# Performance work log

Hardware: AMD Instinct MI355X
Metric: run time of the kernel (lower is better)

Reference implementation:

```python
import jax, jax.numpy as jnp
import numpy as np

B, C, H, W = 16, 64, 1024, 16  # requires C*W == H per the module's implicit view/matmul constraint
C8 = C // 8


def setup_inputs() -> dict:
    key = jax.random.key(0)
    ks = jax.random.split(key, 7)
    s_in = 1.0 / np.sqrt(C)
    return {
        "x": jax.random.normal(ks[0], (B, C, H, W), dtype=jnp.float32),
        "Wq": jax.random.normal(ks[1], (C8, C), dtype=jnp.float32) * s_in,
        "bq": jax.random.normal(ks[2], (C8,), dtype=jnp.float32) * 0.01,
        "Wk": jax.random.normal(ks[3], (C8, C), dtype=jnp.float32) * s_in,
        "bk": jax.random.normal(ks[4], (C8,), dtype=jnp.float32) * 0.01,
        "Wv": jax.random.normal(ks[5], (C, C), dtype=jnp.float32) * s_in,
        "bv": jax.random.normal(ks[6], (C,), dtype=jnp.float32) * 0.01,
    }


def conv1x1(x, w, b):
    # 1x1 conv == per-pixel channel mixing: [B,C,H,W] x [O,C] -> [B,O,H,W]
    return jnp.einsum("bchw,oc->bohw", x, w) + b[None, :, None, None]


def reference(x, Wq, bq, Wk, bk, Wv, bv):
    b, c, h, w = x.shape
    q = conv1x1(x, Wq, bq)  # [B, C/8, H, W]
    k = conv1x1(x, Wk, bk)  # [B, C/8, H, W]
    v = conv1x1(x, Wv, bv)  # [B, C, H, W]
    # Faithful to torch .view(B, -1, H): row-major reshape, NOT a transpose.
    qf = jnp.swapaxes(q.reshape(b, -1, h), 1, 2)  # [B, H, C8*W]
    kf = k.reshape(b, -1, h)                      # [B, C8*W, H]
    vf = v.reshape(b, -1, h)                      # [B, C*W, H] (C*W == H)
    scores = jax.nn.softmax(jnp.matmul(qf, kf), axis=-1)  # [B, H, H]
    attended = jnp.matmul(scores, vf)             # [B, H, H]
    attended = attended.reshape(v.shape)          # [B, C, H, W]
    return x + attended
```

## Files before the change

kernel.cpp:

```cpp
#include <hip/hip_runtime.h>
#include <stdint.h>

typedef uint32_t u32;
typedef __attribute__((ext_vector_type(4))) float f32x4;
typedef __attribute__((ext_vector_type(8))) short short8;

#define NBATCH 16
#define NPIX   16384
#define NPB    1048576

__device__ __forceinline__ ushort f2bf(float f) {
  u32 b = __builtin_bit_cast(u32, f);
  return (ushort)((b + 0x7FFFu + ((b >> 16) & 1u)) >> 16);
}
__device__ __forceinline__ float bf2f(ushort h) {
  return __builtin_bit_cast(float, (u32)h << 16);
}

__device__ __forceinline__ void gload16(const void* g, void* l) {
  __builtin_amdgcn_global_load_lds(
      (const __attribute__((address_space(1))) u32*)g,
      (__attribute__((address_space(3))) u32*)l,
      16, 0, 0);
}

__global__ void prep_w2(const float* __restrict__ Wq, const float* __restrict__ bq,
                        const float* __restrict__ Wk, const float* __restrict__ bk,
                        const float* __restrict__ Wv, const float* __restrict__ bv,
                        ushort* __restrict__ Wpk, float* __restrict__ bpk)
{
  int gid = blockIdx.x * 256 + threadIdx.x;
  if (gid < 12288) {
    int m = gid >> 7, kk = gid & 127;
    int ch = kk & 63;
    ushort outv = 0;
    if (m < 8) {
      float wv = Wq[m * 64 + ch];
      ushort h = f2bf(wv);
      outv = (kk < 64) ? h : f2bf(wv - bf2f(h));
    } else if (m < 16) {
      float wv = Wk[(m - 8) * 64 + ch];
      ushort h = f2bf(wv);
      outv = (kk < 64) ? h : f2bf(wv - bf2f(h));
    } else if (m < 80) {
      outv = (kk < 64) ? f2bf(Wv[(m - 16) * 64 + ch]) : (ushort)0;
    }
    Wpk[gid] = outv;
  } else if (gid < 12368) {
    int o = gid - 12288;
    bpk[o] = (o < 8) ? bq[o] : (o < 16 ? bk[o - 8] : bv[o - 16]);
  }
}

__global__ __launch_bounds__(256) void proj10(
    const float* __restrict__ x, const ushort* __restrict__ Wpk,
    const float* __restrict__ bpk,
    ushort* __restrict__ Qt2, ushort* __restrict__ Kt2,
    ushort* __restrict__ Vt)
{
  __shared__ __align__(16) char smem[32768];
  float* xs = (float*)smem;
  int t = threadIdx.x;
  int w = t >> 6, lane = t & 63;
  int l15 = lane & 15, l4 = lane >> 4;

  int g = blockIdx.x;
  int lin = (g & 7) * 256 + (g >> 3);
  int b = lin >> 7;
  int l0 = (lin & 127) << 3;
  const float* xb = x + (size_t)b * NPB + l0;

  #pragma unroll
  for (int it = 0; it < 8; ++it) {
    int f0 = (it * 4 + w) * 64;
    int f = f0 + lane;
    int ch = f >> 5, r2 = f & 31, tc = r2 >> 1, half = r2 & 1;
    gload16(xb + (size_t)ch * NPIX + tc * 1024 + half * 4, xs + f0 * 4);
  }

  const uint4* Wp4 = (const uint4*)Wpk;
  uint4 Afrag[12];
  #pragma unroll
  for (int kc = 0; kc < 4; ++kc)
    Afrag[kc] = Wp4[l15 * 16 + kc * 4 + l4];
  #pragma unroll
  for (int mt = 1; mt < 5; ++mt)
    #pragma unroll
    for (int kc = 0; kc < 2; ++kc)
      Afrag[2 + mt * 2 + kc] = Wp4[(mt * 16 + l15) * 16 + kc * 4 + l4];

  f32x4 acc[5][2];
  #pragma unroll
  for (int mt = 0; mt < 5; ++mt) {
    f32x4 bv4;
    #pragma unroll
    for (int r = 0; r < 4; ++r) bv4[r] = bpk[mt * 16 + l4 * 4 + r];
    acc[mt][0] = bv4; acc[mt][1] = bv4;
  }

  __syncthreads();

  #pragma unroll
  for (int i = 0; i < 2; ++i) {
    int px = (w * 2 + i) * 16 + l15;
    u32 xr[16];
    #pragma unroll
    for (int kc = 0; kc < 2; ++kc)
      #pragma unroll
      for (int j = 0; j < 8; ++j)
        xr[kc * 8 + j] = ((const u32*)xs)[(kc * 32 + l4 * 8 + j) * 128 + px];
    uint4 bxh[2], bxl[2];
    #pragma unroll
    for (int kc = 0; kc < 2; ++kc)
      #pragma unroll
      for (int p = 0; p < 4; ++p) {
        u32 a = xr[kc * 8 + 2 * p], c = xr[kc * 8 + 2 * p + 1];
        ((u32*)&bxh[kc])[p] = (a >> 16) | (c & 0xFFFF0000u);
        float fa = __builtin_bit_cast(float, a) -
                   __builtin_bit_cast(float, a & 0xFFFF0000u);
        float fc = __builtin_bit_cast(float, c) -
                   __builtin_bit_cast(float, c & 0xFFFF0000u);
        u32 la = __builtin_bit_cast(u32, fa), lc = __builtin_bit_cast(u32, fc);
        ((u32*)&bxl[kc])[p] = (la >> 16) | (lc & 0xFFFF0000u);
      }
    short8 h0 = __builtin_bit_cast(short8, bxh[0]);
    short8 h1 = __builtin_bit_cast(short8, bxh[1]);
    short8 s0 = __builtin_bit_cast(short8, bxl[0]);
    short8 s1 = __builtin_bit_cast(short8, bxl[1]);
    acc[0][i] = __builtin_amdgcn_mfma_f32_16x16x32_bf16(
        __builtin_bit_cast(short8, Afrag[0]), h0, acc[0][i], 0, 0, 0);
    acc[0][i] = __builtin_amdgcn_mfma_f32_16x16x32_bf16(
        __builtin_bit_cast(short8, Afrag[1]), h1, acc[0][i], 0, 0, 0);
    acc[0][i] = __builtin_amdgcn_mfma_f32_16x16x32_bf16(
        __builtin_bit_cast(short8, Afrag[0]), s0, acc[0][i], 0, 0, 0);
    acc[0][i] = __builtin_amdgcn_mfma_f32_16x16x32_bf16(
        __builtin_bit_cast(short8, Afrag[1]), s1, acc[0][i], 0, 0, 0);
    acc[0][i] = __builtin_amdgcn_mfma_f32_16x16x32_bf16(
        __builtin_bit_cast(short8, Afrag[2]), h0, acc[0][i], 0, 0, 0);
    acc[0][i] = __builtin_amdgcn_mfma_f32_16x16x32_bf16(
        __builtin_bit_cast(short8, Afrag[3]), h1, acc[0][i], 0, 0, 0);
    #pragma unroll
    for (int mt = 1; mt < 5; ++mt) {
      acc[mt][i] = __builtin_amdgcn_mfma_f32_16x16x32_bf16(
          __builtin_bit_cast(short8, Afrag[2 + mt * 2]), h0, acc[mt][i], 0, 0, 0);
      acc[mt][i] = __builtin_amdgcn_mfma_f32_16x16x32_bf16(
          __builtin_bit_cast(short8, Afrag[3 + mt * 2]), h1, acc[mt][i], 0, 0, 0);
    }
  }
  __syncthreads();

  float*  qkl = (float*)smem;
  ushort* vl  = (ushort*)(smem + 16 * 132 * 4);
  #pragma unroll
  for (int i = 0; i < 2; ++i) {
    int px = (w * 2 + i) * 16 + l15;
    #pragma unroll
    for (int r = 0; r < 4; ++r)
      qkl[(l4 * 4 + r) * 132 + px] = acc[0][i][r];
    #pragma unroll
    for (int mt = 1; mt < 5; ++mt)
      #pragma unroll
      for (int r = 0; r < 4; ++r)
        vl[((mt - 1) * 16 + l4 * 4 + r) * 136 + px] = f2bf(acc[mt][i][r]);
  }
  __syncthreads();

  if (t < 128) {
    int l = t >> 4, tcc = t & 15;
    size_t lrow = (size_t)b * 1024 + l0 + l;
    int px = tcc * 8 + l;

    union { ushort s[8]; uint4 v; } qh, ql, kh, kl;
    #pragma unroll
    for (int o = 0; o < 8; ++o) {
      float qv = qkl[o * 132 + px];
      ushort h = f2bf(qv);
      qh.s[o] = h; ql.s[o] = f2bf(qv - bf2f(h));
      float kv = qkl[(8 + o) * 132 + px];
      h = f2bf(kv);
      kh.s[o] = h; kl.s[o] = f2bf(kv - bf2f(h));
    }
    ushort* qrow = Qt2 + lrow * 384 + tcc * 8;
    *(uint4*)qrow         = qh.v;
    *(uint4*)(qrow + 128) = ql.v;
    *(uint4*)(qrow + 256) = qh.v;
    ushort* krow = Kt2 + lrow * 384 + tcc * 8;
    *(uint4*)krow         = kh.v;
    *(uint4*)(krow + 128) = kh.v;
    *(uint4*)(krow + 256) = kl.v;

    ushort* vrow = Vt + lrow * 1024;
    #pragma unroll
    for (int it = 0; it < 4; ++it) {
      int c2 = (it << 4) + tcc;
      union { ushort s[16]; uint4 q[2]; } ov;
      #pragma unroll
      for (int tt = 0; tt < 16; ++tt)
        ov.s[tt] = vl[c2 * 136 + tt * 8 + l];
      *(uint4*)(vrow + c2 * 16)     = ov.q[0];
      *(uint4*)(vrow + c2 * 16 + 8) = ov.q[1];
    }
  }
}

template<int KTOT, bool ADDX>
__global__ __launch_bounds__(256) void gemm_nt(
    const ushort* __restrict__ A, int lda,
    const ushort* __restrict__ B, int ldb,
    float* __restrict__ C, const float* __restrict__ X)
{
  __shared__ ushort Asm[128 * 64];
  __shared__ ushort Bsm[128 * 64];
  int t = threadIdx.x;

  int g = blockIdx.x;
  int lin = (g & 7) * 128 + (g >> 3);
  int bz = lin >> 6;
  int by = (lin >> 3) & 7;
  int bx = lin & 7;
  int m0 = by << 7, n0 = bx << 7;

  const ushort* Ab = A + (size_t)bz * 1024 * lda;
  const ushort* Bb = B + (size_t)bz * 1024 * ldb;
  int wid = t >> 6, lane = t & 63;
  int wm = wid >> 1, wn = wid & 1;

  int swc = (t & 7) ^ ((t >> 3) & 7);
  const ushort* pa = Ab + (size_t)(m0 + (t >> 3)) * lda + swc * 8;
  const ushort* pb = Bb + (size_t)(n0 + (t >> 3)) * ldb + swc * 8;
  ushort* la0 = Asm + (size_t)(t >> 6) * 512;
  ushort* lb0 = Bsm + (size_t)(t >> 6) * 512;

  f32x4 acc[4][4] = {};

  for (int k0 = 0; k0 < KTOT; k0 += 64) {
    __syncthreads();
    #pragma unroll
    for (int i = 0; i < 4; ++i)
      gload16(pa + (size_t)i * 32 * lda + k0, la0 + i * 2048);
    #pragma unroll
    for (int i = 0; i < 4; ++i)
      gload16(pb + (size_t)i * 32 * ldb + k0, lb0 + i * 2048);
    __syncthreads();
    #pragma unroll
    for (int kk = 0; kk < 2; ++kk) {
      short8 af[4], bfr[4];
      #pragma unroll
      for (int mi = 0; mi < 4; ++mi) {
        int rr = (wm << 6) + (mi << 4) + (lane & 15);
        af[mi] = __builtin_bit_cast(short8,
            ((const uint4*)Asm)[rr * 8 + ((kk * 4 + (lane >> 4)) ^ (rr & 7))]);
      }
      #pragma unroll
      for (int ni = 0; ni < 4; ++ni) {
        int rr = (wn << 6) + (ni << 4) + (lane & 15);
        bfr[ni] = __builtin_bit_cast(short8,
            ((const uint4*)Bsm)[rr * 8 + ((kk * 4 + (lane >> 4)) ^ (rr & 7))]);
      }
      #pragma unroll
      for (int mi = 0; mi < 4; ++mi)
        #pragma unroll
        for (int ni = 0; ni < 4; ++ni)
          acc[mi][ni] = __builtin_amdgcn_mfma_f32_16x16x32_bf16(
              af[mi], bfr[ni], acc[mi][ni], 0, 0, 0);
    }
  }

  #pragma unroll
  for (int mi = 0; mi < 4; ++mi) {
    int rbase = m0 + (wm << 6) + (mi << 4) + ((lane >> 4) << 2);
    #pragma unroll
    for (int ni = 0; ni < 4; ++ni) {
      int col = n0 + (wn << 6) + (ni << 4) + (lane & 15);
      f32x4 v = acc[mi][ni];
      #pragma unroll
      for (int rr = 0; rr < 4; ++rr) {
        size_t idx = ((size_t)bz * 1024 + rbase + rr) * 1024 + col;
        if (ADDX) C[idx] = v[rr] + X[idx];
        else      C[idx] = v[rr];
      }
    }
  }
}

__global__ __launch_bounds__(256) void softmax_rows(float* __restrict__ S)
{
  size_t rowi = blockIdx.x;
  float* srow = S + rowi * 1024;
  int t = threadIdx.x;
  float4 v = ((const float4*)srow)[t];
  float m = fmaxf(fmaxf(v.x, v.y), fmaxf(v.z, v.w));
  #pragma unroll
  for (int off = 32; off > 0; off >>= 1) m = fmaxf(m, __shfl_xor(m, off));
  __shared__ float red[8];
  int wid = t >> 6, lane = t & 63;
  if (lane == 0) red[wid] = m;
  __syncthreads();
  m = fmaxf(fmaxf(red[0], red[1]), fmaxf(red[2], red[3]));
  float e0 = __expf(v.x - m), e1 = __expf(v.y - m);
  float e2 = __expf(v.z - m), e3 = __expf(v.w - m);
  float s = e0 + e1 + e2 + e3;
  #pragma unroll
  for (int off = 32; off > 0; off >>= 1) s += __shfl_xor(s, off);
  if (lane == 0) red[4 + wid] = s;
  __syncthreads();
  s = red[4] + red[5] + red[6] + red[7];
  float inv = 1.0f / s;
  union { ushort h[4]; uint2 q; } pk;
  pk.h[0] = f2bf(e0 * inv); pk.h[1] = f2bf(e1 * inv);
  pk.h[2] = f2bf(e2 * inv); pk.h[3] = f2bf(e3 * inv);
  ((uint2*)srow)[t] = pk.q;
}

extern "C" void kernel_launch(void* const* d_in, const int* in_sizes, int n_in,
                              void* d_out, int out_size, void* d_ws, size_t ws_size,
                              hipStream_t stream) {
  const float* x  = (const float*)d_in[0];
  const float* Wq = (const float*)d_in[1];
  const float* bq = (const float*)d_in[2];
  const float* Wk = (const float*)d_in[3];
  const float* bk = (const float*)d_in[4];
  const float* Wv = (const float*)d_in[5];
  const float* bv = (const float*)d_in[6];
  float* out = (float*)d_out;

  char* wsb = (char*)d_ws;
  ushort* Qt2 = (ushort*)wsb;
  ushort* Kt2 = (ushort*)(wsb + 12582912);
  ushort* Vt  = (ushort*)(wsb + 25165824);
  float*  S   = (float*)(wsb + 58720256);
  ushort* Wpk = (ushort*)(wsb + 92274688);
  float*  bpk = (float*)(wsb + 92274688 + 24576);

  prep_w2<<<49, 256, 0, stream>>>(Wq, bq, Wk, bk, Wv, bv, Wpk, bpk);
  proj10<<<2048, 256, 0, stream>>>(x, Wpk, bpk, Qt2, Kt2, Vt);
  gemm_nt<384, false><<<1024, 256, 0, stream>>>(Qt2, 384, Kt2, 384, S, nullptr);
  softmax_rows<<<16384, 256, 0, stream>>>(S);
  gemm_nt<1024, true><<<1024, 256, 0, stream>>>((const ushort*)S, 2048, Vt, 1024, out, x);
}
```

Before: 129.7 us.

## Double-buffer LDS tiles in gemm_nt to overlap global loads with MFMA

Allocates two LDS buffers for the A and B tiles and prefetches the next K tile with global_load_lds while MFMAs consume the current one. Each iteration now ends with a single vmcnt wait plus barrier instead of two __syncthreads around the loads. The goal is to hide global-memory latency behind compute. The cost is doubled LDS use (64 KB per block), which may reduce occupancy.

```diff
diff --git a/kernel.cpp b/kernel.cpp
--- a/kernel.cpp
+++ b/kernel.cpp
@@ -209,8 +209,8 @@
     const ushort* __restrict__ B, int ldb,
     float* __restrict__ C, const float* __restrict__ X)
 {
-  __shared__ ushort Asm[128 * 64];
-  __shared__ ushort Bsm[128 * 64];
+  __shared__ ushort Asm[2][128 * 64];
+  __shared__ ushort Bsm[2][128 * 64];
   int t = threadIdx.x;
 
   int g = blockIdx.x;
@@ -228,20 +228,32 @@
   int swc = (t & 7) ^ ((t >> 3) & 7);
   const ushort* pa = Ab + (size_t)(m0 + (t >> 3)) * lda + swc * 8;
   const ushort* pb = Bb + (size_t)(n0 + (t >> 3)) * ldb + swc * 8;
-  ushort* la0 = Asm + (size_t)(t >> 6) * 512;
-  ushort* lb0 = Bsm + (size_t)(t >> 6) * 512;
+  int wb = (t >> 6) * 512;
 
   f32x4 acc[4][4] = {};
-
-  for (int k0 = 0; k0 < KTOT; k0 += 64) {
-    __syncthreads();
-    #pragma unroll
-    for (int i = 0; i < 4; ++i)
-      gload16(pa + (size_t)i * 32 * lda + k0, la0 + i * 2048);
-    #pragma unroll
-    for (int i = 0; i < 4; ++i)
-      gload16(pb + (size_t)i * 32 * ldb + k0, lb0 + i * 2048);
-    __syncthreads();
+  constexpr int NT = KTOT / 64;
+
+  #pragma unroll
+  for (int i = 0; i < 4; ++i)
+    gload16(pa + (size_t)i * 32 * lda, Asm[0] + wb + i * 2048);
+  #pragma unroll
+  for (int i = 0; i < 4; ++i)
+    gload16(pb + (size_t)i * 32 * ldb, Bsm[0] + wb + i * 2048);
+  asm volatile("s_waitcnt vmcnt(0)" ::: "memory");
+  __builtin_amdgcn_s_barrier();
+
+  #pragma unroll 2
+  for (int it = 0; it < NT; ++it) {
+    int cur = it & 1;
+    if (it + 1 < NT) {
+      int k0 = (it + 1) * 64;
+      #pragma unroll
+      for (int i = 0; i < 4; ++i)
+        gload16(pa + (size_t)i * 32 * lda + k0, Asm[cur ^ 1] + wb + i * 2048);
+      #pragma unroll
+      for (int i = 0; i < 4; ++i)
+        gload16(pb + (size_t)i * 32 * ldb + k0, Bsm[cur ^ 1] + wb + i * 2048);
+    }
     #pragma unroll
     for (int kk = 0; kk < 2; ++kk) {
       short8 af[4], bfr[4];
@@ -249,13 +261,13 @@
       for (int mi = 0; mi < 4; ++mi) {
         int rr = (wm << 6) + (mi << 4) + (lane & 15);
         af[mi] = __builtin_bit_cast(short8,
-            ((const uint4*)Asm)[rr * 8 + ((kk * 4 + (lane >> 4)) ^ (rr & 7))]);
+            ((const uint4*)Asm[cur])[rr * 8 + ((kk * 4 + (lane >> 4)) ^ (rr & 7))]);
       }
       #pragma unroll
       for (int ni = 0; ni < 4; ++ni) {
         int rr = (wn << 6) + (ni << 4) + (lane & 15);
         bfr[ni] = __builtin_bit_cast(short8,
-            ((const uint4*)Bsm)[rr * 8 + ((kk * 4 + (lane >> 4)) ^ (rr & 7))]);
+            ((const uint4*)Bsm[cur])[rr * 8 + ((kk * 4 + (lane >> 4)) ^ (rr & 7))]);
       }
       #pragma unroll
       for (int mi = 0; mi < 4; ++mi)
@@ -264,6 +276,8 @@
           acc[mi][ni] = __builtin_amdgcn_mfma_f32_16x16x32_bf16(
               af[mi], bfr[ni], acc[mi][ni], 0, 0, 0);
     }
+    asm volatile("s_waitcnt vmcnt(0)" ::: "memory");
+    __builtin_amdgcn_s_barrier();
   }
 
   #pragma unroll
```

Result: slower. 139.5 us (+7.5%).
